# Performance work log

Measured on AMD Instinct MI355X. Metric: run time of the kernel, lower is better.

The kernel has to match this reference:

```python
import jax, jax.numpy as jnp
import numpy as np

B_, C, N, M, DX = 4, 8, 1024, 1024, 1
POINTS_PER_UNIT = 64


def setup_inputs() -> dict:
    key = jax.random.key(0)
    k1, k2, k3 = jax.random.split(key, 3)
    xz = jax.random.uniform(k1, (M, DX), dtype=jnp.float32)          # grid locations
    z = jax.random.normal(k2, (B_, C, M, M), dtype=jnp.float32)      # grid encoding
    x = jax.random.normal(k3, (B_, N, DX), dtype=jnp.float32)        # target locations
    log_scale = jnp.log(jnp.float32(2.0 / POINTS_PER_UNIT))          # learned scalar
    return {"xz": xz, "z": z, "x": x, "log_scale": log_scale}


def reference(xz, z, x, log_scale):
    # pairwise squared distances: (b, n, m)
    dists2 = jnp.sum((x[:, :, None, :] - xz[None, None, :, :]) ** 2, axis=-1)
    # RBF weights
    weights = jnp.exp(-0.5 * dists2 / jnp.exp(2.0 * log_scale))      # (b, n, m)
    # weighted interpolation of grid encoding: (b, c, n, m)
    z1 = jnp.einsum("bnm,bcmk->bcnk", weights, z)
    # outer product z1 @ z1^T: (b, c, n, n)
    z2 = jnp.einsum("bcnk,bcok->bcno", z1, z1)
    return (xz, z2)
```

## Files before the change

### kernel.cpp

```cpp
#include <hip/hip_runtime.h>
#include <hip/hip_bf16.h>


typedef __attribute__((ext_vector_type(8))) unsigned short u16x8;
typedef __attribute__((ext_vector_type(8))) __bf16 bf16x8;
typedef __attribute__((ext_vector_type(4))) float f32x4;

typedef __attribute__((address_space(1))) void gvoid;
typedef __attribute__((address_space(3))) void svoid;
#define GLDS(g, s) __builtin_amdgcn_global_load_lds((gvoid*)(g), (svoid*)(s), 16, 0, 0)
#define BAR() asm volatile("s_barrier" ::: "memory")

__device__ __forceinline__ unsigned short f2bf(float f) {
  unsigned int u = __builtin_bit_cast(unsigned int, f);
  u += 0x7fffu + ((u >> 16) & 1u);
  return (unsigned short)(u >> 16);
}

__device__ __forceinline__ bf16x8 as_bf16x8(u16x8 v) {
  return __builtin_bit_cast(bf16x8, v);
}

__global__ void weights_kernel(const float* __restrict__ xz, const float* __restrict__ x,
                               const float* __restrict__ ls, unsigned short* __restrict__ W) {
  int bn = blockIdx.x;
  float xv = x[bn];
  float coef = -0.5f * __expf(-2.0f * ls[0]);
  unsigned short* Wrow = W + (size_t)bn * 1024;
  #pragma unroll
  for (int i = 0; i < 4; ++i) {
    int m = threadIdx.x + i * 256;
    float d = xv - xz[m];
    Wrow[m] = f2bf(__expf(coef * d * d));
  }
}

__global__ void transpose_kernel(const float* __restrict__ Z, unsigned short* __restrict__ Zt) {
  __shared__ float tile[64][65];
  int bc = blockIdx.z;
  const float* Zp = Z + ((size_t)bc << 20);
  unsigned short* Ztp = Zt + ((size_t)bc << 20);
  int m0 = blockIdx.x * 64, k0 = blockIdx.y * 64;
  int tx = threadIdx.x & 63, tg = threadIdx.x >> 6;
  #pragma unroll
  for (int i = 0; i < 16; ++i) {
    int ml = tg + i * 4;
    tile[ml][tx] = Zp[(size_t)(m0 + ml) * 1024 + k0 + tx];
  }
  __syncthreads();
  int tx2 = (threadIdx.x & 31) * 2, kg = threadIdx.x >> 5;
  #pragma unroll
  for (int i = 0; i < 8; ++i) {
    int kl = kg + i * 8;
    ushort2 v;
    v.x = f2bf(tile[tx2][kl]);
    v.y = f2bf(tile[tx2 + 1][kl]);
    *(ushort2*)&Ztp[(size_t)(k0 + kl) * 1024 + m0 + tx2] = v;
  }
}

template<bool A_PER_B>
__global__ __launch_bounds__(512, 2)
void gemm_nt8(const unsigned short* __restrict__ A, const unsigned short* __restrict__ B,
              unsigned short* __restrict__ Cbf) {
  extern __shared__ __align__(16) char smem[];

  const int bid = blockIdx.x;
  const int w = ((bid & 7) << 6) + (bid >> 3);
  const int bc = w >> 4;
  const int t  = w & 15;
  const int bi = t & 3, bj = t >> 2;

  const unsigned short* Ap = A + ((size_t)(A_PER_B ? (bc >> 3) : bc) << 20);
  const unsigned short* Bp = B + ((size_t)bc << 20);
  const int tid = threadIdx.x;
  const int wv = tid >> 6, lane = tid & 63;
  const int wr = wv >> 2, wc = wv & 3;
  const int la = lane & 15, ha = lane >> 4;

  f32x4 acc[8][4] = {};

  const int slog = (lane & 7) ^ (lane >> 3);
  const int rloc = 2 * (lane >> 3) + (slog & 1);
  const int cloc = (slog >> 1) * 8;
  const unsigned short* gA0 = Ap + (size_t)(bi*256 +       wv*16 + rloc) * 1024 + cloc;
  const unsigned short* gA1 = Ap + (size_t)(bi*256 + 128 + wv*16 + rloc) * 1024 + cloc;
  const unsigned short* gB0 = Bp + (size_t)(bj*256 +       wv*16 + rloc) * 1024 + cloc;
  const unsigned short* gB1 = Bp + (size_t)(bj*256 + 128 + wv*16 + rloc) * 1024 + cloc;
  const int ldsw = wv * 1024;

  auto stageA = [&](int d, int kh, int kt) {
    const int ko = kt * 64 + kh * 32;
    char* dst = smem + d * 32768 + kh * 16384 + ldsw;
    GLDS(gA0 + ko, dst); GLDS(gA1 + ko, dst + 8192);
  };
  auto stageB = [&](int d, int kh, int kt) {
    const int ko = kt * 64 + kh * 32;
    char* dst = smem + 65536 + d * 32768 + kh * 16384 + ldsw;
    GLDS(gB0 + ko, dst); GLDS(gB1 + ko, dst + 8192);
  };

  const int sphys = ((ha << 1) | (la & 1)) ^ (la >> 1);
  const int abase = wr * 8192 + (la >> 1) * 128 + sphys * 16;
  const int bbase = 65536 + wc * 4096 + (la >> 1) * 128 + sphys * 16;

  u16x8 aX[4], aY[4], b0[4], b1[4];
  auto lda4 = [&](u16x8* dst, int d, int kh, int ms) {
    const char* p = smem + d * 32768 + kh * 16384 + ms * 4096 + abase;
    dst[0] = *(const u16x8*)(p);
    dst[1] = *(const u16x8*)(p + 1024);
    dst[2] = *(const u16x8*)(p + 2048);
    dst[3] = *(const u16x8*)(p + 3072);
  };
  auto ldb4 = [&](u16x8* dst, int d, int kh) {
    const char* p = smem + d * 32768 + kh * 16384 + bbase;
    dst[0] = *(const u16x8*)(p);
    dst[1] = *(const u16x8*)(p + 1024);
    dst[2] = *(const u16x8*)(p + 2048);
    dst[3] = *(const u16x8*)(p + 3072);
  };
  auto mfma16 = [&](const u16x8* Af, const u16x8* Bf, int ms) {
    #pragma unroll
    for (int i = 0; i < 4; ++i)
      #pragma unroll
      for (int n = 0; n < 4; ++n)
        acc[ms * 4 + i][n] = __builtin_amdgcn_mfma_f32_16x16x32_bf16(
            as_bf16x8(Af[i]), as_bf16x8(Bf[n]), acc[ms * 4 + i][n], 0, 0, 0);
  };

  stageA(0, 0, 0); stageB(0, 0, 0);
  stageA(0, 1, 0); stageB(0, 1, 0);
  stageA(1, 0, 1); stageB(1, 0, 1);
  asm volatile("s_waitcnt vmcnt(8)" ::: "memory");
  BAR();
  ldb4(b0, 0, 0); lda4(aX, 0, 0, 0);

  for (int tt = 0; tt < 14; ++tt) {
    const int d = tt & 1;
    stageA(d ^ 1, 1, tt + 1);
    lda4(aY, d, 0, 1);
    mfma16(aX, b0, 0);
    stageB(d ^ 1, 1, tt + 1);
    asm volatile("s_waitcnt vmcnt(8)" ::: "memory");
    BAR();
    ldb4(b1, d, 1); lda4(aX, d, 1, 0);
    mfma16(aY, b0, 1);
    stageA(d, 0, tt + 2);
    lda4(aY, d, 1, 1);
    mfma16(aX, b1, 0);
    stageB(d, 0, tt + 2);
    asm volatile("s_waitcnt vmcnt(8)" ::: "memory");
    BAR();
    ldb4(b0, d ^ 1, 0); lda4(aX, d ^ 1, 0, 0);
    mfma16(aY, b1, 1);
  }
  stageA(1, 1, 15);
  lda4(aY, 0, 0, 1);
  mfma16(aX, b0, 0);
  stageB(1, 1, 15);
  asm volatile("s_waitcnt vmcnt(8)" ::: "memory");
  BAR();
  ldb4(b1, 0, 1); lda4(aX, 0, 1, 0);
  mfma16(aY, b0, 1);
  lda4(aY, 0, 1, 1);
  mfma16(aX, b1, 0);
  asm volatile("s_waitcnt vmcnt(4)" ::: "memory");
  BAR();
  ldb4(b0, 1, 0); lda4(aX, 1, 0, 0);
  mfma16(aY, b1, 1);
  lda4(aY, 1, 0, 1);
  mfma16(aX, b0, 0);
  asm volatile("s_waitcnt vmcnt(0)" ::: "memory");
  BAR();
  ldb4(b1, 1, 1); lda4(aX, 1, 1, 0);
  mfma16(aY, b0, 1);
  lda4(aY, 1, 1, 1);
  mfma16(aX, b1, 0);
  mfma16(aY, b1, 1);
  BAR();

  const size_t cb20 = (size_t)bc << 20;
  unsigned short* sE = (unsigned short*)(smem) + wv * 1152;
  const int r2 = lane >> 2, ch = lane & 3;
  #pragma unroll
  for (int mb = 0; mb < 8; ++mb) {
    #pragma unroll
    for (int nb = 0; nb < 4; ++nb)
      #pragma unroll
      for (int j = 0; j < 4; ++j)
        sE[(ha * 4 + j) * 72 + nb * 16 + la] = f2bf(acc[mb][nb][j]);
    u16x8 v0 = *(const u16x8*)&sE[r2 * 72 + ch * 16];
    u16x8 v1 = *(const u16x8*)&sE[r2 * 72 + ch * 16 + 8];
    unsigned short* gp = Cbf + cb20 +
        (size_t)(bi * 256 + wr * 128 + mb * 16 + r2) * 1024 + bj * 256 + wc * 64 + ch * 16;
    *(u16x8*)gp = v0;
    *(u16x8*)(gp + 8) = v1;
  }
}

__global__ __launch_bounds__(256, 3)
void gemm2_sym(const unsigned short* __restrict__ A, float* __restrict__ Cf) {
  __shared__ __align__(16) char smem[49152];

  const int chunk = 144;
  int w = ((int)blockIdx.x & 7) * chunk + ((int)blockIdx.x >> 3);
  int bc = w / 36;
  int t  = w % 36;
  int bi = 0;
  while (t >= 8 - bi) { t -= 8 - bi; ++bi; }
  int bj = bi + t;

  const unsigned short* Ap = A + ((size_t)bc << 20);
  const int tid = threadIdx.x;
  const int wave = tid >> 6, lane = tid & 63;
  const int wr = wave >> 1, wc = wave & 1;
  const int la = lane & 15, ha = lane >> 4;
  f32x4 acc[4][4] = {};

  const int slog = (lane & 7) ^ ((lane >> 3) & 7);
  const int rloc = 2 * (lane >> 3) + (slog & 1);
  const int cloc = (slog >> 1) * 8;
  const unsigned short* gA0 = Ap + (size_t)(bi * 128 + (wave * 2)     * 16 + rloc) * 1024 + cloc;
  const unsigned short* gA1 = Ap + (size_t)(bi * 128 + (wave * 2 + 1) * 16 + rloc) * 1024 + cloc;
  const unsigned short* gB0 = Ap + (size_t)(bj * 128 + (wave * 2)     * 16 + rloc) * 1024 + cloc;
  const unsigned short* gB1 = Ap + (size_t)(bj * 128 + (wave * 2 + 1) * 16 + rloc) * 1024 + cloc;

  auto stage = [&](int slot, int kt) {
    char* dA = smem + slot * 8192 + wave * 2048;
    char* dB = smem + 24576 + slot * 8192 + wave * 2048;
    GLDS(gA0 + kt, dA); GLDS(gA1 + kt, dA + 1024);
    GLDS(gB0 + kt, dB); GLDS(gB1 + kt, dB + 1024);
  };

  const int sphys = ((ha << 1) | (la & 1)) ^ (la >> 1);
  const int aoff = wr * 4096 + (la >> 1) * 128 + sphys * 16;
  const int boff = 24576 + wc * 4096 + (la >> 1) * 128 + sphys * 16;

  u16x8 aX[4], bX[4], aY[4], bY[4];
  auto rd = [&](u16x8* da, u16x8* db, int slot) {
    const char* pa = smem + slot * 8192 + aoff;
    const char* pb = smem + slot * 8192 + boff;
    da[0] = *(const u16x8*)(pa);
    da[1] = *(const u16x8*)(pa + 1024);
    da[2] = *(const u16x8*)(pa + 2048);
    da[3] = *(const u16x8*)(pa + 3072);
    db[0] = *(const u16x8*)(pb);
    db[1] = *(const u16x8*)(pb + 1024);
    db[2] = *(const u16x8*)(pb + 2048);
    db[3] = *(const u16x8*)(pb + 3072);
  };
  auto mfma16 = [&](const u16x8* Af, const u16x8* Bf) {
    __builtin_amdgcn_s_setprio(1);
    #pragma unroll
    for (int m = 0; m < 4; ++m)
      #pragma unroll
      for (int n = 0; n < 4; ++n)
        acc[m][n] = __builtin_amdgcn_mfma_f32_16x16x32_bf16(
            as_bf16x8(Af[m]), as_bf16x8(Bf[n]), acc[m][n], 0, 0, 0);
    __builtin_amdgcn_s_setprio(0);
  };

  stage(0, 0); stage(1, 32); stage(2, 64);
  asm volatile("s_waitcnt vmcnt(4)" ::: "memory");
  BAR();
  rd(aX, bX, 0);
  asm volatile("s_waitcnt lgkmcnt(0)" ::: "memory");
  BAR();

  int p0 = 0, p1 = 1, p2 = 2;
  for (int t2 = 0; t2 < 28; t2 += 2) {
    stage(p0, (t2 + 3) * 32);
    rd(aY, bY, p1);
    mfma16(aX, bX);
    asm volatile("s_waitcnt vmcnt(4)" ::: "memory");
    BAR();
    stage(p1, (t2 + 4) * 32);
    rd(aX, bX, p2);
    mfma16(aY, bY);
    asm volatile("s_waitcnt vmcnt(4)" ::: "memory");
    BAR();
    int tmp = p2; p2 = p1; p1 = p0; p0 = tmp;
  }
  stage(p0, 31 * 32);
  rd(aY, bY, p1);
  mfma16(aX, bX);
  asm volatile("s_waitcnt vmcnt(4)" ::: "memory");
  BAR();
  rd(aX, bX, p2);
  mfma16(aY, bY);
  asm volatile("s_waitcnt vmcnt(0)" ::: "memory");
  BAR();
  rd(aY, bY, p0);
  mfma16(aX, bX);
  mfma16(aY, bY);
  BAR();

  const size_t cb20 = (size_t)bc << 20;

  #pragma unroll
  for (int m = 0; m < 4; ++m) {
    int row0 = bi * 128 + wr * 64 + m * 16 + ha * 4;
    #pragma unroll
    for (int n = 0; n < 4; ++n) {
      int col = bj * 128 + wc * 64 + n * 16 + la;
      #pragma unroll
      for (int j = 0; j < 4; ++j)
        Cf[cb20 + (size_t)(row0 + j) * 1024 + col] = acc[m][n][j];
    }
  }
  if (bi != bj) {
    float (*sT)[129] = (float(*)[129])smem;
    #pragma unroll
    for (int b = 0; b < 4; ++b) {
      if (wr == (b >> 1)) {
        #pragma unroll
        for (int dm = 0; dm < 2; ++dm) {
          int m = (b & 1) * 2 + dm;
          #pragma unroll
          for (int n = 0; n < 4; ++n)
            #pragma unroll
            for (int j = 0; j < 4; ++j)
              sT[dm * 16 + ha * 4 + j][wc * 64 + n * 16 + la] = acc[m][n][j];
        }
      }
      __syncthreads();
      int c  = tid >> 1;
      int r0 = (tid & 1) * 16;
      float* gp = Cf + cb20 + (size_t)(bj * 128 + c) * 1024 + bi * 128 + b * 32 + r0;
      #pragma unroll
      for (int q = 0; q < 4; ++q) {
        f32x4 v;
        #pragma unroll
        for (int k = 0; k < 4; ++k) v[k] = sT[r0 + q * 4 + k][c];
        *(f32x4*)(gp + q * 4) = v;
      }
      __syncthreads();
    }
  }
}

extern "C" void kernel_launch(void* const* d_in, const int* in_sizes, int n_in,
                              void* d_out, int out_size, void* d_ws, size_t ws_size,
                              hipStream_t stream) {
  const float* xz = (const float*)d_in[0];
  const float* z  = (const float*)d_in[1];
  const float* x  = (const float*)d_in[2];
  const float* ls = (const float*)d_in[3];
  float* out = (float*)d_out;

  unsigned short* W  = (unsigned short*)d_ws;
  unsigned short* Zt = W + ((size_t)4 << 20);
  unsigned short* z1 = Zt + ((size_t)32 << 20);

  hipFuncSetAttribute((const void*)gemm_nt8<true>,
                      hipFuncAttributeMaxDynamicSharedMemorySize, 131072);

  hipMemcpyAsync(out, xz, 1024 * sizeof(float), hipMemcpyDeviceToDevice, stream);
  weights_kernel<<<4096, 256, 0, stream>>>(xz, x, ls, W);
  transpose_kernel<<<dim3(16, 16, 32), 256, 0, stream>>>(z, Zt);
  gemm_nt8<true><<<512, 512, 131072, stream>>>(W, Zt, z1);
  gemm2_sym<<<32 * 36, 256, 0, stream>>>(z1, out + 1024);
}
```

Measured before the change: 171.3 us.

## Restructure gemm2_sym pipeline to double-buffered 64-wide K stages with split halves

Replaces the triple-buffered 32-wide K ring in the symmetric z1·z1ᵀ GEMM with a double buffer of 64-wide K tiles, each split into two 32-wide halves staged and consumed in an interleaved order. Shared memory becomes dynamic at 64 KB and launch bounds drop from 3 to 2 blocks per CU. The aim is fewer barriers per K-step and more loads in flight per wave to hide global latency, at the cost of lower occupancy. The vmcnt waits and the tail handling are rewritten to match the new stage order.

```diff
diff --git a/kernel.cpp b/kernel.cpp
--- a/kernel.cpp
+++ b/kernel.cpp
@@ -198,9 +198,9 @@
   }
 }
 
-__global__ __launch_bounds__(256, 3)
+__global__ __launch_bounds__(256, 2)
 void gemm2_sym(const unsigned short* __restrict__ A, float* __restrict__ Cf) {
-  __shared__ __align__(16) char smem[49152];
+  extern __shared__ __align__(16) char smem[];
 
   const int chunk = 144;
   int w = ((int)blockIdx.x & 7) * chunk + ((int)blockIdx.x >> 3);
@@ -217,37 +217,43 @@
   const int la = lane & 15, ha = lane >> 4;
   f32x4 acc[4][4] = {};
 
-  const int slog = (lane & 7) ^ ((lane >> 3) & 7);
+  const int slog = (lane & 7) ^ (lane >> 3);
   const int rloc = 2 * (lane >> 3) + (slog & 1);
   const int cloc = (slog >> 1) * 8;
-  const unsigned short* gA0 = Ap + (size_t)(bi * 128 + (wave * 2)     * 16 + rloc) * 1024 + cloc;
-  const unsigned short* gA1 = Ap + (size_t)(bi * 128 + (wave * 2 + 1) * 16 + rloc) * 1024 + cloc;
-  const unsigned short* gB0 = Ap + (size_t)(bj * 128 + (wave * 2)     * 16 + rloc) * 1024 + cloc;
-  const unsigned short* gB1 = Ap + (size_t)(bj * 128 + (wave * 2 + 1) * 16 + rloc) * 1024 + cloc;
-
-  auto stage = [&](int slot, int kt) {
-    char* dA = smem + slot * 8192 + wave * 2048;
-    char* dB = smem + 24576 + slot * 8192 + wave * 2048;
-    GLDS(gA0 + kt, dA); GLDS(gA1 + kt, dA + 1024);
-    GLDS(gB0 + kt, dB); GLDS(gB1 + kt, dB + 1024);
+  const unsigned short* gA0 = Ap + (size_t)(bi*128 + (wave*2  )*16 + rloc)*1024 + cloc;
+  const unsigned short* gA1 = Ap + (size_t)(bi*128 + (wave*2+1)*16 + rloc)*1024 + cloc;
+  const unsigned short* gB0 = Ap + (size_t)(bj*128 + (wave*2  )*16 + rloc)*1024 + cloc;
+  const unsigned short* gB1 = Ap + (size_t)(bj*128 + (wave*2+1)*16 + rloc)*1024 + cloc;
+  const int ldsw = wave * 2048;
+
+  auto stageA = [&](int d, int kh, int kt) {
+    const int ko = kt * 64 + kh * 32;
+    char* dst = smem + d * 32768 + kh * 8192 + ldsw;
+    GLDS(gA0 + ko, dst); GLDS(gA1 + ko, dst + 1024);
+  };
+  auto stageB = [&](int d, int kh, int kt) {
+    const int ko = kt * 64 + kh * 32;
+    char* dst = smem + d * 32768 + 16384 + kh * 8192 + ldsw;
+    GLDS(gB0 + ko, dst); GLDS(gB1 + ko, dst + 1024);
   };
 
   const int sphys = ((ha << 1) | (la & 1)) ^ (la >> 1);
-  const int aoff = wr * 4096 + (la >> 1) * 128 + sphys * 16;
-  const int boff = 24576 + wc * 4096 + (la >> 1) * 128 + sphys * 16;
+  const int inv = (la >> 1) * 128 + sphys * 16;
 
   u16x8 aX[4], bX[4], aY[4], bY[4];
-  auto rd = [&](u16x8* da, u16x8* db, int slot) {
-    const char* pa = smem + slot * 8192 + aoff;
-    const char* pb = smem + slot * 8192 + boff;
-    da[0] = *(const u16x8*)(pa);
-    da[1] = *(const u16x8*)(pa + 1024);
-    da[2] = *(const u16x8*)(pa + 2048);
-    da[3] = *(const u16x8*)(pa + 3072);
-    db[0] = *(const u16x8*)(pb);
-    db[1] = *(const u16x8*)(pb + 1024);
-    db[2] = *(const u16x8*)(pb + 2048);
-    db[3] = *(const u16x8*)(pb + 3072);
+  auto lda4 = [&](u16x8* dst, int d, int kh) {
+    const char* p = smem + d * 32768 + kh * 8192 + wr * 4096 + inv;
+    dst[0] = *(const u16x8*)(p);
+    dst[1] = *(const u16x8*)(p + 1024);
+    dst[2] = *(const u16x8*)(p + 2048);
+    dst[3] = *(const u16x8*)(p + 3072);
+  };
+  auto ldb4 = [&](u16x8* dst, int d, int kh) {
+    const char* p = smem + d * 32768 + 16384 + kh * 8192 + wc * 4096 + inv;
+    dst[0] = *(const u16x8*)(p);
+    dst[1] = *(const u16x8*)(p + 1024);
+    dst[2] = *(const u16x8*)(p + 2048);
+    dst[3] = *(const u16x8*)(p + 3072);
   };
   auto mfma16 = [&](const u16x8* Af, const u16x8* Bf) {
     __builtin_amdgcn_s_setprio(1);
@@ -260,38 +266,39 @@
     __builtin_amdgcn_s_setprio(0);
   };
 
-  stage(0, 0); stage(1, 32); stage(2, 64);
+  stageA(0, 0, 0); stageB(0, 0, 0);
+  stageA(0, 1, 0); stageB(0, 1, 0);
+  stageA(1, 0, 1); stageB(1, 0, 1);
+  asm volatile("s_waitcnt vmcnt(8)" ::: "memory");
+  BAR();
+  lda4(aX, 0, 0); ldb4(bX, 0, 0);
+
+  for (int tt = 0; tt < 14; ++tt) {
+    const int d = tt & 1, e = d ^ 1;
+    stageA(e, 1, tt + 1); stageB(e, 1, tt + 1);
+    mfma16(aX, bX);
+    asm volatile("s_waitcnt vmcnt(8)" ::: "memory");
+    BAR();
+    lda4(aY, d, 1); ldb4(bY, d, 1);
+    stageA(d, 0, tt + 2); stageB(d, 0, tt + 2);
+    mfma16(aY, bY);
+    asm volatile("s_waitcnt vmcnt(8)" ::: "memory");
+    BAR();
+    lda4(aX, e, 0); ldb4(bX, e, 0);
+  }
+  stageA(1, 1, 15); stageB(1, 1, 15);
+  mfma16(aX, bX);
+  asm volatile("s_waitcnt vmcnt(8)" ::: "memory");
+  BAR();
+  lda4(aY, 0, 1); ldb4(bY, 0, 1);
+  mfma16(aY, bY);
   asm volatile("s_waitcnt vmcnt(4)" ::: "memory");
   BAR();
-  rd(aX, bX, 0);
-  asm volatile("s_waitcnt lgkmcnt(0)" ::: "memory");
-  BAR();
-
-  int p0 = 0, p1 = 1, p2 = 2;
-  for (int t2 = 0; t2 < 28; t2 += 2) {
-    stage(p0, (t2 + 3) * 32);
-    rd(aY, bY, p1);
-    mfma16(aX, bX);
-    asm volatile("s_waitcnt vmcnt(4)" ::: "memory");
-    BAR();
-    stage(p1, (t2 + 4) * 32);
-    rd(aX, bX, p2);
-    mfma16(aY, bY);
-    asm volatile("s_waitcnt vmcnt(4)" ::: "memory");
-    BAR();
-    int tmp = p2; p2 = p1; p1 = p0; p0 = tmp;
-  }
-  stage(p0, 31 * 32);
-  rd(aY, bY, p1);
+  lda4(aX, 1, 0); ldb4(bX, 1, 0);
   mfma16(aX, bX);
-  asm volatile("s_waitcnt vmcnt(4)" ::: "memory");
-  BAR();
-  rd(aX, bX, p2);
-  mfma16(aY, bY);
   asm volatile("s_waitcnt vmcnt(0)" ::: "memory");
   BAR();
-  rd(aY, bY, p0);
-  mfma16(aX, bX);
+  lda4(aY, 1, 1); ldb4(bY, 1, 1);
   mfma16(aY, bY);
   BAR();
 
@@ -354,10 +361,12 @@
 
   hipFuncSetAttribute((const void*)gemm_nt8<true>,
                       hipFuncAttributeMaxDynamicSharedMemorySize, 131072);
+  hipFuncSetAttribute((const void*)gemm2_sym,
+                      hipFuncAttributeMaxDynamicSharedMemorySize, 65536);
 
   hipMemcpyAsync(out, xz, 1024 * sizeof(float), hipMemcpyDeviceToDevice, stream);
   weights_kernel<<<4096, 256, 0, stream>>>(xz, x, ls, W);
   transpose_kernel<<<dim3(16, 16, 32), 256, 0, stream>>>(z, Zt);
   gemm_nt8<true><<<512, 512, 131072, stream>>>(W, Zt, z1);
-  gemm2_sym<<<32 * 36, 256, 0, stream>>>(z1, out + 1024);
-}
+  gemm2_sym<<<32 * 36, 256, 65536, stream>>>(z1, out + 1024);
+}
```

New measurement: 172.3 us. About the same (+0.6%).
